# Kernel optimization log

Measured on AMD Instinct MI355X. Metric: run time of the kernel, lower is better.

The kernel has to match this reference:

```python
import jax, jax.numpy as jnp
import numpy as np

INPUT, HIDDEN, LAYERS = 512, 1024, 2
BATCH, SEQ = 64, 512


def _gru_layer(x, h0, W_ih, W_hh, b_ih, b_hh):
    """Run one GRU layer over time. x: [B,T,D_in], h0: [B,H] -> (out [B,T,H], h_T [B,H])."""
    H = h0.shape[-1]
    # Input-side gates are time-independent: precompute as one big GEMM.
    gi = jnp.einsum('btd,gd->btg', x, W_ih) + b_ih  # [B,T,3H]

    def step(h, gi_t):
        gh = h @ W_hh.T + b_hh                      # [B,3H]
        i_r, i_z, i_n = jnp.split(gi_t, 3, axis=1)
        h_r, h_z, h_n = jnp.split(gh, 3, axis=1)
        r = jax.nn.sigmoid(i_r + h_r)
        z = jax.nn.sigmoid(i_z + h_z)
        n = jnp.tanh(i_n + r * h_n)
        h_new = (1 - z) * h + z * n
        return h_new, h_new

    h_T, out = jax.lax.scan(step, h0, jnp.swapaxes(gi, 0, 1))  # scan over time
    return jnp.swapaxes(out, 0, 1), h_T


def setup_inputs() -> dict:
    key = jax.random.key(0)
    ks = jax.random.split(key, 8)
    stdv = 1.0 / np.sqrt(HIDDEN)

    def u(k, shape):
        return jax.random.uniform(k, shape, jnp.float32, -stdv, stdv)

    return {
        'x': jax.random.normal(ks[0], (BATCH, SEQ, INPUT), jnp.float32),
        'h0': jnp.zeros((LAYERS, BATCH, HIDDEN), jnp.float32),
        'W_ih0': u(ks[1], (3 * HIDDEN, INPUT)),
        'W_hh0': u(ks[2], (3 * HIDDEN, HIDDEN)),
        'b_ih0': jnp.zeros((3 * HIDDEN,), jnp.float32),
        'b_hh0': jnp.zeros((3 * HIDDEN,), jnp.float32),
        'W_ih1': u(ks[3], (3 * HIDDEN, HIDDEN)),
        'W_hh1': u(ks[4], (3 * HIDDEN, HIDDEN)),
        'b_ih1': jnp.zeros((3 * HIDDEN,), jnp.float32),
        'b_hh1': jnp.zeros((3 * HIDDEN,), jnp.float32),
    }


def reference(x, h0, W_ih0, W_hh0, b_ih0, b_hh0, W_ih1, W_hh1, b_ih1, b_hh1):
    # Layer-by-layer is mathematically identical to the per-timestep interleaved
    # loop in the torch code (layer l at time t depends only on layer l-1 up to t).
    out0, hT0 = _gru_layer(x, h0[0], W_ih0, W_hh0, b_ih0, b_hh0)
    out1, hT1 = _gru_layer(out0, h0[1], W_ih1, W_hh1, b_ih1, b_hh1)
    h_n = jnp.stack([hT0, hT1])  # [num_layers, B, H]
    return out1, h_n
```

## Files before the change

kernel.cpp:

```cpp
#include <hip/hip_runtime.h>
#include <math.h>

#define HID  1024
#define SEQ  512
#define NB   64
#define DIN0 512

using short8 = __attribute__((ext_vector_type(8))) short;
using f32x4  = __attribute__((ext_vector_type(4))) float;

__device__ __forceinline__ unsigned short f2bf(float f) {
    unsigned int u = __float_as_uint(f);
    u += 0x7fffu + ((u >> 16) & 1u);
    return (unsigned short)(u >> 16);
}
__device__ __forceinline__ float sigm_(float x) { return 1.0f / (1.0f + __expf(-x)); }
__device__ __forceinline__ float tanh_(float x) {
    float ax = fabsf(x);
    float e = __expf(-2.0f * ax);
    float t = (1.0f - e) / (1.0f + e);
    return copysignf(t, x);
}

__device__ __forceinline__ void ld_coh(short8* a, const unsigned short* p) {
    asm volatile("global_load_dwordx4 %0, %1, off sc0 sc1" : "=&v"(*a) : "v"(p) : "memory");
}
__device__ __forceinline__ void ld_pln(short8* a, const unsigned short* p) {
    asm volatile("global_load_dwordx4 %0, %1, off" : "=&v"(*a) : "v"(p) : "memory");
}
__device__ __forceinline__ void st_coh_u16(unsigned short* p, unsigned short v) {
    asm volatile("global_store_short %0, %1, off sc0 sc1" :: "v"(p), "v"((unsigned)v) : "memory");
}

template<int LAYER>
__device__ __forceinline__ void gru_loop(
    const unsigned short* __restrict__ xb,
    const unsigned short* __restrict__ Wi, const unsigned short* __restrict__ Wh,
    const float* __restrict__ bi, const float* __restrict__ bh_,
    const float* __restrict__ h0f,
    unsigned short* __restrict__ hb,
    float* out,
    unsigned* __restrict__ bar, int bid, float (*lds)[2][16][68])
{
    constexpr int Din = LAYER ? HID : DIN0;
    constexpr int K   = Din + HID;
    constexpr int Kq  = K / 8;
    constexpr int NK  = Kq / 32;

    const int q   = bid & 127;
    const int j0  = (q >> 1) << 4;
    const int b0  = (q & 1) << 5;
    const int tid = threadIdx.x;
    const int l   = tid & 63;
    const int w   = tid >> 6;
    const int c   = l & 15;
    const int kg  = l >> 4;
    const int kq0 = w * Kq;

    unsigned* gens  = bar;
    unsigned* flags = bar + 128;

    short8 Br[NK], Bz[NK], Bn[NK];
#pragma unroll
    for (int s = 0; s < NK; ++s) {
        const int k0 = kq0 + s * 32 + kg * 8;
        const unsigned short *pr, *pz, *pn;
        if (k0 < Din) {
            pr = Wi + (long)(j0 + c) * Din + k0;
            pz = Wi + (long)(HID + j0 + c) * Din + k0;
            pn = Wi + (long)(2 * HID + j0 + c) * Din + k0;
        } else {
            pr = Wh + (long)(j0 + c) * HID + (k0 - Din);
            pz = Wh + (long)(HID + j0 + c) * HID + (k0 - Din);
            pn = Wh + (long)(2 * HID + j0 + c) * HID + (k0 - Din);
        }
        Br[s] = *(const short8*)pr;
        Bz[s] = *(const short8*)pz;
        Bn[s] = *(const short8*)pn;
    }

    const long hrow0 = (long)(b0 + c) * HID;
    const long hrow1 = (long)(b0 + 16 + c) * HID;
    const long xrow0 = (long)(b0 + c) * SEQ * DIN0;
    const long xrow1 = (long)(b0 + 16 + c) * SEQ * DIN0;

    const int cb  = tid >> 4;
    const int jc  = tid & 15;
    const int cm  = cb >> 4, cbr = cb & 15;
    const int j   = j0 + jc;
    const int bgl = b0 + cb;
    const float bir = bi[j], biz = bi[HID + j], bin = bi[2 * HID + j];
    const float bhr = bh_[j], bhz = bh_[HID + j], bhn = bh_[2 * HID + j];
    float hreg = h0f[LAYER * 65536 + bgl * 1024 + j];

    for (int i = 0; i <= SEQ; ++i) {
        const int st = LAYER ? (i - 1) : i;
        if (st >= 0 && st < SEQ) {
            const int rp = st & 1, wp = rp ^ 1;
            const unsigned short* Alo = hb + (long)(0 * 2 + wp) * NB * HID;
            const unsigned short* Ahi = hb + (long)(LAYER * 2 + rp) * NB * HID;
            const unsigned short* xp0 = xb + xrow0 + (long)st * DIN0;
            const unsigned short* xp1 = xb + xrow1 + (long)st * DIN0;

            f32x4 acc_r[2], acc_z[2], acc_nx[2], acc_nh[2];
#pragma unroll
            for (int m = 0; m < 2; ++m) {
                acc_r[m] = (f32x4){0.f, 0.f, 0.f, 0.f};
                acc_z[m] = (f32x4){0.f, 0.f, 0.f, 0.f};
                acc_nx[m] = (f32x4){0.f, 0.f, 0.f, 0.f};
                acc_nh[m] = (f32x4){0.f, 0.f, 0.f, 0.f};
            }

            short8 abuf[NK][2];

#define ISSUE(g) do {                                                          \
    const int kk_ = kq0 + (g) * 32 + kg * 8;                                   \
    const bool lo_ = (kq0 + (g) * 32) < Din;                                   \
    if (LAYER == 0) {                                                          \
        if (lo_) { ld_pln(&abuf[g][0], xp0 + kk_);                             \
                   ld_pln(&abuf[g][1], xp1 + kk_); }                           \
        else     { ld_coh(&abuf[g][0], Ahi + hrow0 + (kk_ - Din));             \
                   ld_coh(&abuf[g][1], Ahi + hrow1 + (kk_ - Din)); }           \
    } else {                                                                   \
        const unsigned short* bse_ = lo_ ? (Alo + kk_) : (Ahi + (kk_ - HID));  \
        ld_coh(&abuf[g][0], bse_ + hrow0);                                     \
        ld_coh(&abuf[g][1], bse_ + hrow1);                                     \
    } } while (0)

#define WSTEP(s, W) do {                                                                               \
    asm volatile("s_waitcnt vmcnt(" #W ")" ::: "memory");                                              \
    __builtin_amdgcn_sched_barrier(0);                                                                 \
    const bool lo_ = (kq0 + (s) * 32) < Din;                                                           \
    acc_r[0] = __builtin_amdgcn_mfma_f32_16x16x32_bf16(abuf[s][0], Br[s], acc_r[0], 0, 0, 0);          \
    acc_r[1] = __builtin_amdgcn_mfma_f32_16x16x32_bf16(abuf[s][1], Br[s], acc_r[1], 0, 0, 0);          \
    acc_z[0] = __builtin_amdgcn_mfma_f32_16x16x32_bf16(abuf[s][0], Bz[s], acc_z[0], 0, 0, 0);          \
    acc_z[1] = __builtin_amdgcn_mfma_f32_16x16x32_bf16(abuf[s][1], Bz[s], acc_z[1], 0, 0, 0);          \
    if (lo_) {                                                                                         \
        acc_nx[0] = __builtin_amdgcn_mfma_f32_16x16x32_bf16(abuf[s][0], Bn[s], acc_nx[0], 0, 0, 0);    \
        acc_nx[1] = __builtin_amdgcn_mfma_f32_16x16x32_bf16(abuf[s][1], Bn[s], acc_nx[1], 0, 0, 0);    \
    } else {                                                                                           \
        acc_nh[0] = __builtin_amdgcn_mfma_f32_16x16x32_bf16(abuf[s][0], Bn[s], acc_nh[0], 0, 0, 0);    \
        acc_nh[1] = __builtin_amdgcn_mfma_f32_16x16x32_bf16(abuf[s][1], Bn[s], acc_nh[1], 0, 0, 0);    \
    } } while (0)

            if constexpr (NK == 8) {
                ISSUE(0); ISSUE(1); ISSUE(2); ISSUE(3);
                ISSUE(4); ISSUE(5); ISSUE(6); ISSUE(7);
                WSTEP(0, 14); WSTEP(1, 12); WSTEP(2, 10); WSTEP(3, 8);
                WSTEP(4, 6);  WSTEP(5, 4);  WSTEP(6, 2);  WSTEP(7, 0);
            } else {
                ISSUE(0); ISSUE(1); ISSUE(2);
                ISSUE(3); ISSUE(4); ISSUE(5);
                WSTEP(0, 10); WSTEP(1, 8); WSTEP(2, 6);
                WSTEP(3, 4);  WSTEP(4, 2); WSTEP(5, 0);
            }
#undef ISSUE
#undef WSTEP

#pragma unroll
            for (int m = 0; m < 2; ++m)
#pragma unroll
                for (int v = 0; v < 4; ++v) {
                    f32x4 pk = { acc_r[m][v], acc_z[m][v], acc_nx[m][v], acc_nh[m][v] };
                    *(f32x4*)&lds[w][m][kg * 4 + v][c * 4] = pk;
                }
            __syncthreads();

            float rr = 0.f, zz = 0.f, nx = 0.f, nh = 0.f;
#pragma unroll
            for (int ww = 0; ww < 8; ++ww) {
                f32x4 g = *(const f32x4*)&lds[ww][cm][cbr][jc * 4];
                rr += g[0]; zz += g[1]; nx += g[2]; nh += g[3];
            }
            const float r = sigm_(rr + bir + bhr);
            const float z = sigm_(zz + biz + bhz);
            const float n = tanh_((nx + bin) + r * (nh + bhn));
            const float hnew = (1.f - z) * hreg + z * n;
            hreg = hnew;
            const long nofs = ((long)(LAYER * 2 + ((st & 1) ^ 1)) * NB + bgl) * HID + j;
            st_coh_u16(hb + nofs, f2bf(hnew));
            if (LAYER) out[((long)bgl * SEQ + st) * HID + j] = hnew;
            if (st == SEQ - 1)
                out[(long)NB * SEQ * HID + LAYER * 65536 + bgl * 1024 + j] = hnew;
        }

        if (i == SEQ) break;

        asm volatile("s_waitcnt vmcnt(0)" ::: "memory");
        __syncthreads();
        const unsigned tgt = (unsigned)(i + 1);
        if (tid == 0)
            __hip_atomic_store(flags + bid, tgt, __ATOMIC_RELAXED, __HIP_MEMORY_SCOPE_AGENT);
        if (bid == 0) {
            if (tid < 64) {
                bool ok;
                do {
                    unsigned f0 = __hip_atomic_load(flags + tid,       __ATOMIC_RELAXED, __HIP_MEMORY_SCOPE_AGENT);
                    unsigned f1 = __hip_atomic_load(flags + 64 + tid,  __ATOMIC_RELAXED, __HIP_MEMORY_SCOPE_AGENT);
                    unsigned f2 = __hip_atomic_load(flags + 128 + tid, __ATOMIC_RELAXED, __HIP_MEMORY_SCOPE_AGENT);
                    unsigned f3 = __hip_atomic_load(flags + 192 + tid, __ATOMIC_RELAXED, __HIP_MEMORY_SCOPE_AGENT);
                    ok = (f0 >= tgt) & (f1 >= tgt) & (f2 >= tgt) & (f3 >= tgt);
                } while (!__all(ok));
                if (tid < 8)
                    __hip_atomic_store(gens + tid * 16, tgt, __ATOMIC_RELAXED, __HIP_MEMORY_SCOPE_AGENT);
            }
            __syncthreads();
        } else {
            if (tid == 0) {
                while (__hip_atomic_load(gens + (bid & 7) * 16, __ATOMIC_RELAXED, __HIP_MEMORY_SCOPE_AGENT) < tgt)
                    __builtin_amdgcn_s_sleep(2);
            }
            __syncthreads();
        }
    }
}

__global__ __launch_bounds__(512, 2) void gru_persist(
    const unsigned short* __restrict__ xb,
    const unsigned short* __restrict__ W0i, const unsigned short* __restrict__ W0h,
    const unsigned short* __restrict__ W1i, const unsigned short* __restrict__ W1h,
    const float* __restrict__ bi0, const float* __restrict__ bh0,
    const float* __restrict__ bi1, const float* __restrict__ bh1,
    const float* __restrict__ h0f, unsigned short* __restrict__ hb,
    float* out, unsigned* __restrict__ bar)
{
    __shared__ float lds[8][2][16][68];
    const int bid = blockIdx.x;
    if (bid < 128) gru_loop<0>(xb, W0i, W0h, bi0, bh0, h0f, hb, out, bar, bid, lds);
    else           gru_loop<1>(xb, W1i, W1h, bi1, bh1, h0f, hb, out, bar, bid, lds);
}

__global__ __launch_bounds__(256) void cvt_bf16(const float* __restrict__ src,
                                                unsigned short* __restrict__ dst, int n4) {
    int i = blockIdx.x * 256 + threadIdx.x;
    if (i >= n4) return;
    float4 f = *(const float4*)(src + 4L * i);
    unsigned long long u =  (unsigned long long)f2bf(f.x)
                         | ((unsigned long long)f2bf(f.y) << 16)
                         | ((unsigned long long)f2bf(f.z) << 32)
                         | ((unsigned long long)f2bf(f.w) << 48);
    *(unsigned long long*)(dst + 4L * i) = u;
}

__global__ __launch_bounds__(256) void init_h(const float* __restrict__ h0,
                                              unsigned short* __restrict__ hb) {
    int i = blockIdx.x * 256 + threadIdx.x;
    int layer = i >> 16, idx = i & 65535;
    hb[(long)(layer * 2 + 0) * 65536 + idx] = f2bf(h0[i]);
}

extern "C" void kernel_launch(void* const* d_in, const int* in_sizes, int n_in,
                              void* d_out, int out_size, void* d_ws, size_t ws_size,
                              hipStream_t stream) {
    const float* x    = (const float*)d_in[0];
    const float* h0   = (const float*)d_in[1];
    const float* Wih0 = (const float*)d_in[2];
    const float* Whh0 = (const float*)d_in[3];
    const float* bih0 = (const float*)d_in[4];
    const float* bhh0 = (const float*)d_in[5];
    const float* Wih1 = (const float*)d_in[6];
    const float* Whh1 = (const float*)d_in[7];
    const float* bih1 = (const float*)d_in[8];
    const float* bhh1 = (const float*)d_in[9];

    float* out = (float*)d_out;

    unsigned short* W0i = (unsigned short*)d_ws;
    unsigned short* W0h = W0i + 3072L * 512;
    unsigned short* W1i = W0h + 3072L * 1024;
    unsigned short* W1h = W1i + 3072L * 1024;
    unsigned short* hb  = W1h + 3072L * 1024;
    unsigned*       bar = (unsigned*)(hb + 4L * 65536);
    unsigned short* xb  = (unsigned short*)(bar + 512);

    hipMemsetAsync(bar, 0, 2048, stream);

    cvt_bf16<<<(3072 * 512 / 4  + 255) / 256, 256, 0, stream>>>(Wih0, W0i, 3072 * 512 / 4);
    cvt_bf16<<<(3072 * 1024 / 4 + 255) / 256, 256, 0, stream>>>(Whh0, W0h, 3072 * 1024 / 4);
    cvt_bf16<<<(3072 * 1024 / 4 + 255) / 256, 256, 0, stream>>>(Wih1, W1i, 3072 * 1024 / 4);
    cvt_bf16<<<(3072 * 1024 / 4 + 255) / 256, 256, 0, stream>>>(Whh1, W1h, 3072 * 1024 / 4);
    cvt_bf16<<<(NB * SEQ * DIN0 / 4 + 255) / 256, 256, 0, stream>>>(x, xb, NB * SEQ * DIN0 / 4);
    init_h<<<512, 256, 0, stream>>>(h0, hb);

    gru_persist<<<256, 512, 0, stream>>>(xb, W0i, W0h, W1i, W1h,
                                         bih0, bhh0, bih1, bhh1,
                                         h0, hb, out, bar);
}
```

Baseline: 3.432 ms.

## Replace centralized grid barrier with per-batch-half dataflow flags and deeper h buffering

Removes the global barrier where block 0 gathers all 256 flags and broadcasts a generation counter. Each block now publishes its own progress flag and polls only the 64 flags of its batch half for layer 0 and layer 1. Layer 0 gets a 4-deep bf16 hidden-state ring so it can run up to two steps ahead of layer 1, while layer 1 keeps a double buffer. This cuts barrier latency and lets the two layers run loosely coupled, at the cost of more polling traffic and more delicate buffer-reuse correctness.

```diff
diff --git a/kernel.cpp b/kernel.cpp
--- a/kernel.cpp
+++ b/kernel.cpp
@@ -38,7 +38,7 @@
     const unsigned short* __restrict__ Wi, const unsigned short* __restrict__ Wh,
     const float* __restrict__ bi, const float* __restrict__ bh_,
     const float* __restrict__ h0f,
-    unsigned short* __restrict__ hb,
+    unsigned short* __restrict__ hb0, unsigned short* __restrict__ hb1,
     float* out,
     unsigned* __restrict__ bar, int bid, float (*lds)[2][16][68])
 {
@@ -47,18 +47,21 @@
     constexpr int Kq  = K / 8;
     constexpr int NK  = Kq / 32;
 
-    const int q   = bid & 127;
-    const int j0  = (q >> 1) << 4;
-    const int b0  = (q & 1) << 5;
-    const int tid = threadIdx.x;
-    const int l   = tid & 63;
-    const int w   = tid >> 6;
-    const int c   = l & 15;
-    const int kg  = l >> 4;
-    const int kq0 = w * Kq;
-
-    unsigned* gens  = bar;
-    unsigned* flags = bar + 128;
+    const int q    = bid & 127;
+    const int jsl  = q >> 1;
+    const int j0   = jsl << 4;
+    const int beta = q & 1;
+    const int b0   = beta << 5;
+    const int tid  = threadIdx.x;
+    const int l    = tid & 63;
+    const int w    = tid >> 6;
+    const int c    = l & 15;
+    const int kg   = l >> 4;
+    const int kq0  = w * Kq;
+
+    const unsigned* pA = bar + beta * 64;
+    const unsigned* pB = bar + 128 + beta * 64;
+    unsigned* myflag = (unsigned*)(LAYER ? pB : pA) + jsl;
 
     short8 Br[NK], Bz[NK], Bn[NK];
 #pragma unroll
@@ -94,11 +97,25 @@
     float hreg = h0f[LAYER * 65536 + bgl * 1024 + j];
 
     for (int i = 0; i <= SEQ; ++i) {
+        if (LAYER == 0 && i == SEQ) break;
+
+        if (tid < 64) {
+            const int thrA = i;
+            const int thrB = LAYER ? i : (i - 2);
+            for (;;) {
+                int a = (int)__hip_atomic_load(pA + tid, __ATOMIC_RELAXED, __HIP_MEMORY_SCOPE_AGENT);
+                int b = (int)__hip_atomic_load(pB + tid, __ATOMIC_RELAXED, __HIP_MEMORY_SCOPE_AGENT);
+                if (__all((a >= thrA) & (b >= thrB))) break;
+                __builtin_amdgcn_s_sleep(2);
+            }
+        }
+        __syncthreads();
+
         const int st = LAYER ? (i - 1) : i;
         if (st >= 0 && st < SEQ) {
-            const int rp = st & 1, wp = rp ^ 1;
-            const unsigned short* Alo = hb + (long)(0 * 2 + wp) * NB * HID;
-            const unsigned short* Ahi = hb + (long)(LAYER * 2 + rp) * NB * HID;
+            const unsigned short* Alo = hb0 + (long)(st & 3) * 65536;
+            const unsigned short* Ahi = LAYER ? hb1 + (long)(st & 1) * 65536
+                                              : hb0 + (long)((st + 3) & 3) * 65536;
             const unsigned short* xp0 = xb + xrow0 + (long)st * DIN0;
             const unsigned short* xp1 = xb + xrow1 + (long)st * DIN0;
 
@@ -177,8 +194,9 @@
             const float n = tanh_((nx + bin) + r * (nh + bhn));
             const float hnew = (1.f - z) * hreg + z * n;
             hreg = hnew;
-            const long nofs = ((long)(LAYER * 2 + ((st & 1) ^ 1)) * NB + bgl) * HID + j;
-            st_coh_u16(hb + nofs, f2bf(hnew));
+            unsigned short* stw = LAYER ? hb1 + (long)((st & 1) ^ 1) * 65536
+                                        : hb0 + (long)(st & 3) * 65536;
+            st_coh_u16(stw + (long)bgl * HID + j, f2bf(hnew));
             if (LAYER) out[((long)bgl * SEQ + st) * HID + j] = hnew;
             if (st == SEQ - 1)
                 out[(long)NB * SEQ * HID + LAYER * 65536 + bgl * 1024 + j] = hnew;
@@ -188,30 +206,8 @@
 
         asm volatile("s_waitcnt vmcnt(0)" ::: "memory");
         __syncthreads();
-        const unsigned tgt = (unsigned)(i + 1);
         if (tid == 0)
-            __hip_atomic_store(flags + bid, tgt, __ATOMIC_RELAXED, __HIP_MEMORY_SCOPE_AGENT);
-        if (bid == 0) {
-            if (tid < 64) {
-                bool ok;
-                do {
-                    unsigned f0 = __hip_atomic_load(flags + tid,       __ATOMIC_RELAXED, __HIP_MEMORY_SCOPE_AGENT);
-                    unsigned f1 = __hip_atomic_load(flags + 64 + tid,  __ATOMIC_RELAXED, __HIP_MEMORY_SCOPE_AGENT);
-                    unsigned f2 = __hip_atomic_load(flags + 128 + tid, __ATOMIC_RELAXED, __HIP_MEMORY_SCOPE_AGENT);
-                    unsigned f3 = __hip_atomic_load(flags + 192 + tid, __ATOMIC_RELAXED, __HIP_MEMORY_SCOPE_AGENT);
-                    ok = (f0 >= tgt) & (f1 >= tgt) & (f2 >= tgt) & (f3 >= tgt);
-                } while (!__all(ok));
-                if (tid < 8)
-                    __hip_atomic_store(gens + tid * 16, tgt, __ATOMIC_RELAXED, __HIP_MEMORY_SCOPE_AGENT);
-            }
-            __syncthreads();
-        } else {
-            if (tid == 0) {
-                while (__hip_atomic_load(gens + (bid & 7) * 16, __ATOMIC_RELAXED, __HIP_MEMORY_SCOPE_AGENT) < tgt)
-                    __builtin_amdgcn_s_sleep(2);
-            }
-            __syncthreads();
-        }
+            __hip_atomic_store(myflag, (unsigned)(i + 1), __ATOMIC_RELAXED, __HIP_MEMORY_SCOPE_AGENT);
     }
 }
 
@@ -221,13 +217,14 @@
     const unsigned short* __restrict__ W1i, const unsigned short* __restrict__ W1h,
     const float* __restrict__ bi0, const float* __restrict__ bh0,
     const float* __restrict__ bi1, const float* __restrict__ bh1,
-    const float* __restrict__ h0f, unsigned short* __restrict__ hb,
+    const float* __restrict__ h0f,
+    unsigned short* __restrict__ hb0, unsigned short* __restrict__ hb1,
     float* out, unsigned* __restrict__ bar)
 {
     __shared__ float lds[8][2][16][68];
     const int bid = blockIdx.x;
-    if (bid < 128) gru_loop<0>(xb, W0i, W0h, bi0, bh0, h0f, hb, out, bar, bid, lds);
-    else           gru_loop<1>(xb, W1i, W1h, bi1, bh1, h0f, hb, out, bar, bid, lds);
+    if (bid < 128) gru_loop<0>(xb, W0i, W0h, bi0, bh0, h0f, hb0, hb1, out, bar, bid, lds);
+    else           gru_loop<1>(xb, W1i, W1h, bi1, bh1, h0f, hb0, hb1, out, bar, bid, lds);
 }
 
 __global__ __launch_bounds__(256) void cvt_bf16(const float* __restrict__ src,
@@ -243,10 +240,12 @@
 }
 
 __global__ __launch_bounds__(256) void init_h(const float* __restrict__ h0,
-                                              unsigned short* __restrict__ hb) {
+                                              unsigned short* __restrict__ hb0,
+                                              unsigned short* __restrict__ hb1) {
     int i = blockIdx.x * 256 + threadIdx.x;
-    int layer = i >> 16, idx = i & 65535;
-    hb[(long)(layer * 2 + 0) * 65536 + idx] = f2bf(h0[i]);
+    float v = h0[i];
+    if (i < 65536) hb0[3L * 65536 + i] = f2bf(v);
+    else           hb1[(long)(i - 65536)] = f2bf(v);
 }
 
 extern "C" void kernel_launch(void* const* d_in, const int* in_sizes, int n_in,
@@ -269,8 +268,9 @@
     unsigned short* W0h = W0i + 3072L * 512;
     unsigned short* W1i = W0h + 3072L * 1024;
     unsigned short* W1h = W1i + 3072L * 1024;
-    unsigned short* hb  = W1h + 3072L * 1024;
-    unsigned*       bar = (unsigned*)(hb + 4L * 65536);
+    unsigned short* hb0 = W1h + 3072L * 1024;
+    unsigned short* hb1 = hb0 + 4L * 65536;
+    unsigned*       bar = (unsigned*)(hb1 + 2L * 65536);
     unsigned short* xb  = (unsigned short*)(bar + 512);
 
     hipMemsetAsync(bar, 0, 2048, stream);
@@ -280,9 +280,9 @@
     cvt_bf16<<<(3072 * 1024 / 4 + 255) / 256, 256, 0, stream>>>(Wih1, W1i, 3072 * 1024 / 4);
     cvt_bf16<<<(3072 * 1024 / 4 + 255) / 256, 256, 0, stream>>>(Whh1, W1h, 3072 * 1024 / 4);
     cvt_bf16<<<(NB * SEQ * DIN0 / 4 + 255) / 256, 256, 0, stream>>>(x, xb, NB * SEQ * DIN0 / 4);
-    init_h<<<512, 256, 0, stream>>>(h0, hb);
+    init_h<<<512, 256, 0, stream>>>(h0, hb0, hb1);
 
     gru_persist<<<256, 512, 0, stream>>>(xb, W0i, W0h, W1i, W1h,
                                          bih0, bhh0, bih1, bhh1,
-                                         h0, hb, out, bar);
-}
+                                         h0, hb0, hb1, out, bar);
+}
```

After: 4.176 ms. 1.22x slower.
